# Performance work log

Measured on AMD Instinct MI355X. Metric: run time of the kernel, lower is better.

Reference implementation:

```python
import jax, jax.numpy as jnp
import numpy as np

COMMITMENT_COST = 0.25
NUM_EMBEDDINGS = 512
EMBEDDING_DIM = 64


def setup_inputs() -> dict:
    key = jax.random.key(0)
    k1, k2 = jax.random.split(key)
    inputs = jax.random.normal(k1, (64, EMBEDDING_DIM, 32, 32), dtype=jnp.float32)
    # nn.Embedding init: uniform(-1/K, 1/K)
    emb_w = jax.random.uniform(
        k2, (NUM_EMBEDDINGS, EMBEDDING_DIM), dtype=jnp.float32,
        minval=-1.0 / NUM_EMBEDDINGS, maxval=1.0 / NUM_EMBEDDINGS)
    return {"inputs": inputs, "emb_w": emb_w}


def reference(inputs, emb_w):
    sg = jax.lax.stop_gradient
    # NCHW -> NHWC
    x = jnp.transpose(inputs, (0, 2, 3, 1))          # [B, H, W, D]
    B, H, W, D = x.shape
    flat = x.reshape(-1, D)                          # [N, D]
    dist = (jnp.sum(flat * flat, axis=1, keepdims=True)
            + jnp.sum(emb_w * emb_w, axis=1)
            - 2.0 * jnp.dot(flat, emb_w.T))          # [N, K]
    idx = jnp.argmin(dist, axis=1)                   # [N]
    # one-hot @ emb_w is just a gather
    quantized = emb_w[idx].reshape(B, H, W, D)       # [B, H, W, D]
    e_latent_loss = jnp.mean((sg(quantized) - x) ** 2)
    q_latent_loss = jnp.mean((quantized - sg(x)) ** 2)
    loss = q_latent_loss + COMMITMENT_COST * e_latent_loss
    # straight-through estimator
    quantized_st = x + sg(quantized - x)
    out = jnp.transpose(quantized_st, (0, 3, 1, 2))  # back to NCHW
    return loss, out, idx[:, None]
```

## Files before the change

kernel.cpp:

```cpp
#include <hip/hip_runtime.h>


#define D_    64
#define HW_   1024
#define N_    65536
#define K_    512
#define M_    128
#define CH_   128
#define NCH_  4
#define NDTOT (N_ * K_ / 8)
#define SVST  132

__global__ __launch_bounds__(256, 2) void vq_main_kernel(const float* __restrict__ inp,
                                                         const float* __restrict__ emb,
                                                         float* __restrict__ out) {
    __shared__ float lds[17156];
    float* ldsx = lds;
    float* ldse = lds + 8192;
    float* nrm  = lds + 16384;
    float* sxs  = lds + 16896;
    int*   fi   = (int*)(lds + 17024);
    float* partial = lds + 17152;

    const int tid  = threadIdx.x;
    const int lane = tid & 63;
    const int wv   = tid >> 6;
    const int pg = (lane & 7) | ((wv & 1) << 3);
    const int kg = ((lane >> 3) & 7) | ((wv >> 1) << 3);

    const int n0  = blockIdx.x * M_;
    const int b   = n0 >> 10;
    const int hw0 = n0 & 1023;
    const float* xbase = inp + b * (D_ * HW_) + hw0;

#pragma unroll
    for (int i = 0; i < 8; ++i) {
        int q  = i * 256 + tid;
        int d  = q >> 5;
        int pq = q & 31;
        float4 v = *(const float4*)(xbase + d * HW_ + pq * 4);
        *(float4*)(ldsx + d * M_ + pq * 4) = v;
    }

#pragma unroll
    for (int h = 0; h < 2; ++h) {
        int k = h * 256 + tid;
        const float* e = emb + k * D_;
        float r[8];
#pragma unroll
        for (int j = 0; j < 8; ++j) r[j] = __fmul_rn(e[j], e[j]);
#pragma unroll
        for (int i = 1; i < 8; ++i)
#pragma unroll
            for (int j = 0; j < 8; ++j)
                r[j] = __fadd_rn(r[j], __fmul_rn(e[i * 8 + j], e[i * 8 + j]));
        nrm[k] = __fadd_rn(__fadd_rn(__fadd_rn(r[0], r[1]), __fadd_rn(r[2], r[3])),
                           __fadd_rn(__fadd_rn(r[4], r[5]), __fadd_rn(r[6], r[7])));
    }
    __syncthreads();

    if (tid < M_) {
        float r[8];
#pragma unroll
        for (int j = 0; j < 8; ++j) {
            float v = ldsx[j * M_ + tid];
            r[j] = __fmul_rn(v, v);
        }
#pragma unroll
        for (int i = 1; i < 8; ++i)
#pragma unroll
            for (int j = 0; j < 8; ++j) {
                float v = ldsx[(i * 8 + j) * M_ + tid];
                r[j] = __fadd_rn(r[j], __fmul_rn(v, v));
            }
        sxs[tid] = __fadd_rn(__fadd_rn(__fadd_rn(r[0], r[1]), __fadd_rn(r[2], r[3])),
                             __fadd_rn(__fadd_rn(r[4], r[5]), __fadd_rn(r[6], r[7])));
    }
    __syncthreads();

    float sxp[8];
#pragma unroll
    for (int pp = 0; pp < 8; ++pp) sxp[pp] = sxs[pg * 8 + pp];

    float runv[8];
    int   runi[8];
#pragma unroll
    for (int pp = 0; pp < 8; ++pp) { runv[pp] = 3.4e38f; runi[pp] = 0; }

    for (int c = 0; c < NCH_; ++c) {
        __syncthreads();
#pragma unroll
        for (int i = 0; i < 8; ++i) {
            int q  = i * 256 + tid;
            int kl = q & 127;
            int dq = q >> 7;
            float4 v = *(const float4*)(emb + (c * CH_ + kl) * D_ + dq * 4);
            ldse[(dq * 4 + 0) * CH_ + kl] = v.x;
            ldse[(dq * 4 + 1) * CH_ + kl] = v.y;
            ldse[(dq * 4 + 2) * CH_ + kl] = v.z;
            ldse[(dq * 4 + 3) * CH_ + kl] = v.w;
        }
        __syncthreads();

        float acc[8][8];
#pragma unroll
        for (int pp = 0; pp < 8; ++pp)
#pragma unroll
            for (int kk = 0; kk < 8; ++kk) acc[pp][kk] = 0.f;

#pragma unroll 2
        for (int d = 0; d < D_; ++d) {
            float4 xa = *(const float4*)(ldsx + d * M_ + pg * 8);
            float4 xb = *(const float4*)(ldsx + d * M_ + pg * 8 + 4);
            float4 ea = *(const float4*)(ldse + d * CH_ + kg * 8);
            float4 eb = *(const float4*)(ldse + d * CH_ + kg * 8 + 4);
            float xr[8] = {xa.x, xa.y, xa.z, xa.w, xb.x, xb.y, xb.z, xb.w};
            float er[8] = {ea.x, ea.y, ea.z, ea.w, eb.x, eb.y, eb.z, eb.w};
#pragma unroll
            for (int pp = 0; pp < 8; ++pp)
#pragma unroll
                for (int kk = 0; kk < 8; ++kk)
                    acc[pp][kk] = fmaf(xr[pp], er[kk], acc[pp][kk]);
        }

#pragma unroll
        for (int pp = 0; pp < 8; ++pp) {
            float sx = sxp[pp];
#pragma unroll
            for (int kk = 0; kk < 8; ++kk) {
                float nk = nrm[c * CH_ + kg * 8 + kk];
                float t1 = __fadd_rn(sx, nk);
                float v  = __fadd_rn(t1, -2.0f * acc[pp][kk]);
                if (v < runv[pp]) { runv[pp] = v; runi[pp] = c * CH_ + kg * 8 + kk; }
            }
        }
    }

    __syncthreads();
    float* sv = ldse;
    int*   si = (int*)(ldse + 16 * SVST);
#pragma unroll
    for (int pp = 0; pp < 8; ++pp) {
        sv[kg * SVST + pg * 8 + pp] = runv[pp];
        si[kg * SVST + pg * 8 + pp] = runi[pp];
    }
    __syncthreads();
    if (tid < M_) {
        float bv = 3.4e38f; int bi = 0x7fffffff;
#pragma unroll
        for (int g = 0; g < 16; ++g) {
            float v  = sv[g * SVST + tid];
            int   ii = si[g * SVST + tid];
            if (v < bv || (v == bv && ii < bi)) { bv = v; bi = ii; }
        }
        fi[tid] = bi;
        out[1 + NDTOT + n0 + tid] = (float)bi;
    }
    __syncthreads();

    const int h = tid >> 7;
    const int p = tid & 127;
    const int idx = fi[p];
    const float4* erow = (const float4*)(emb + idx * D_) + h * 8;
    float* obase = out + 1 + b * (D_ * HW_) + hw0 + p;
    float local = 0.f;
#pragma unroll
    for (int j = 0; j < 8; ++j) {
        float4 e4 = erow[j];
        int d0 = h * 32 + j * 4;
        float ev[4] = {e4.x, e4.y, e4.z, e4.w};
#pragma unroll
        for (int cc = 0; cc < 4; ++cc) {
            float xv = ldsx[(d0 + cc) * M_ + p];
            float df = ev[cc] - xv;
            local = fmaf(df, df, local);
            obase[(d0 + cc) * HW_] = ev[cc];
        }
    }
#pragma unroll
    for (int off = 32; off > 0; off >>= 1)
        local += __shfl_down(local, off, 64);
    if ((tid & 63) == 0) partial[tid >> 6] = local;
    __syncthreads();
    if (tid == 0) {
        float t = partial[0] + partial[1] + partial[2] + partial[3];
        atomicAdd(out, t * (1.25f / (float)NDTOT));
    }
}

extern "C" void kernel_launch(void* const* d_in, const int* in_sizes, int n_in,
                              void* d_out, int out_size, void* d_ws, size_t ws_size,
                              hipStream_t stream) {
    const float* inp = (const float*)d_in[0];
    const float* emb = (const float*)d_in[1];
    float* out = (float*)d_out;

    hipMemsetAsync(d_out, 0, sizeof(float), stream);
    vq_main_kernel<<<512, 256, 0, stream>>>(inp, emb, out);
}
```

Baseline: 138.5 us.

## Compute VQ distances with split-bf16 MFMA and refine near-ties exactly in fp32

Replaces the scalar fp32 FMA distance GEMM with bf16 MFMA 16x16x32 instructions. Inputs and codebook are split into hi/lo bf16 pairs (three products per tile) to approximate fp32 accuracy. A second MFMA pass finds candidate codes within a small margin of the approximate minimum and re-evaluates them with exact fp32 dot products, merged through 64-bit atomicCAS keys so the argmin matches the reference. Codebook fragments and norms are precomputed by two small prep kernels into device globals. This costs extra launches, a doubled MFMA pass, and a correctness dependence on the margin heuristic.

Result: faster. 133.6 us (-3.5%).

```diff
diff --git a/kernel.cpp b/kernel.cpp
--- a/kernel.cpp
+++ b/kernel.cpp
@@ -1,168 +1,281 @@
 #include <hip/hip_runtime.h>
 
 
-#define D_    64
-#define HW_   1024
-#define N_    65536
-#define K_    512
-#define M_    128
-#define CH_   128
-#define NCH_  4
-#define NDTOT (N_ * K_ / 8)
-#define SVST  132
+#define D_     64
+#define HW_    1024
+#define N_     65536
+#define K_     512
+#define NDTOT  4194304
+#define MARGIN 2e-4f
+
+typedef short v8s __attribute__((ext_vector_type(8)));
+typedef float v4f __attribute__((ext_vector_type(4)));
+
+__device__ float g_wsn[K_];
+__device__ short g_frag[K_ * D_ * 2];
+
+__device__ __forceinline__ unsigned short bf16rn(float f) {
+    unsigned int u = __float_as_uint(f);
+    u += 0x7fffu + ((u >> 16) & 1u);
+    return (unsigned short)(u >> 16);
+}
+__device__ __forceinline__ float bf16tof(unsigned short h) {
+    return __uint_as_float(((unsigned int)h) << 16);
+}
+
+__device__ __forceinline__ void exact_min(const float* xcolp, const float* __restrict__ emb,
+                                          int k, float sx, unsigned long long* keyp) {
+    const float* e = emb + k * D_;
+    float dot = 0.f;
+#pragma unroll 8
+    for (int d = 0; d < D_; ++d)
+        dot = fmaf(xcolp[d * HW_], e[d], dot);
+    float t1 = __fadd_rn(sx, g_wsn[k]);
+    float v  = fmaf(-2.0f, dot, t1);
+    unsigned long long nv =
+        (((unsigned long long)__float_as_uint(v)) << 32) | (unsigned int)k;
+    unsigned long long old = *keyp;
+    while (nv < old) {
+        unsigned long long assumed = old;
+        old = atomicCAS(keyp, assumed, nv);
+        if (old == assumed) break;
+    }
+}
+
+__global__ __launch_bounds__(256) void vq_prep_norm(const float* __restrict__ emb,
+                                                    float* __restrict__ out) {
+    int k = blockIdx.x * 256 + threadIdx.x;
+    if (k == 0) out[0] = 0.f;
+    if (k < K_) {
+        const float* e = emb + k * D_;
+        float r[8];
+#pragma unroll
+        for (int j = 0; j < 8; ++j) r[j] = __fmul_rn(e[j], e[j]);
+#pragma unroll
+        for (int i = 1; i < 8; ++i)
+#pragma unroll
+            for (int j = 0; j < 8; ++j)
+                r[j] = __fadd_rn(r[j], __fmul_rn(e[i * 8 + j], e[i * 8 + j]));
+        g_wsn[k] = __fadd_rn(__fadd_rn(__fadd_rn(r[0], r[1]), __fadd_rn(r[2], r[3])),
+                             __fadd_rn(__fadd_rn(r[4], r[5]), __fadd_rn(r[6], r[7])));
+    }
+}
+
+__global__ __launch_bounds__(256) void vq_prep_frag(const float* __restrict__ emb) {
+    const int t = blockIdx.x;
+    const int tid = threadIdx.x;
+    const int s = tid >> 7;
+    const int hl = (tid >> 6) & 1;
+    const int lane = tid & 63;
+    const int c = lane & 15, q = lane >> 4;
+    const float* e = emb + (t * 16 + c) * D_ + s * 32 + q * 8;
+    unsigned int u[4];
+#pragma unroll
+    for (int jp = 0; jp < 4; ++jp) {
+        float f0 = e[jp * 2], f1 = e[jp * 2 + 1];
+        unsigned short h0, h1;
+        if (hl == 0) { h0 = bf16rn(f0); h1 = bf16rn(f1); }
+        else {
+            h0 = bf16rn(f0 - bf16tof(bf16rn(f0)));
+            h1 = bf16rn(f1 - bf16tof(bf16rn(f1)));
+        }
+        u[jp] = (unsigned int)h0 | ((unsigned int)h1 << 16);
+    }
+    ((uint4*)g_frag)[(t * 4 + s * 2 + hl) * 64 + lane] =
+        make_uint4(u[0], u[1], u[2], u[3]);
+}
 
 __global__ __launch_bounds__(256, 2) void vq_main_kernel(const float* __restrict__ inp,
                                                          const float* __restrict__ emb,
                                                          float* __restrict__ out) {
-    __shared__ float lds[17156];
-    float* ldsx = lds;
-    float* ldse = lds + 8192;
-    float* nrm  = lds + 16384;
-    float* sxs  = lds + 16896;
-    int*   fi   = (int*)(lds + 17024);
-    float* partial = lds + 17152;
-
-    const int tid  = threadIdx.x;
+    __shared__ __align__(16) char smem[35344];
+    float* ldsx = (float*)smem;
+    v8s*   ldsB = (v8s*)smem;
+    float* sxs  = (float*)(smem + 32768);
+    float* m_   = (float*)(smem + 33280);
+    int*   ai_  = (int*)(smem + 33792);
+    unsigned long long* key_ = (unsigned long long*)(smem + 34304);
+    float* partial = (float*)(smem + 35328);
+
+    const int tid = threadIdx.x;
     const int lane = tid & 63;
-    const int wv   = tid >> 6;
-    const int pg = (lane & 7) | ((wv & 1) << 3);
-    const int kg = ((lane >> 3) & 7) | ((wv >> 1) << 3);
-
-    const int n0  = blockIdx.x * M_;
-    const int b   = n0 >> 10;
+    const int w = tid >> 6;
+    const int c = lane & 15, q = lane >> 4;
+
+    const int n0 = blockIdx.x * 128;
+    const int b = n0 >> 10;
     const int hw0 = n0 & 1023;
-    const float* xbase = inp + b * (D_ * HW_) + hw0;
+    const float* xg = inp + b * (D_ * HW_) + hw0;
 
 #pragma unroll
     for (int i = 0; i < 8; ++i) {
-        int q  = i * 256 + tid;
-        int d  = q >> 5;
-        int pq = q & 31;
-        float4 v = *(const float4*)(xbase + d * HW_ + pq * 4);
-        *(float4*)(ldsx + d * M_ + pq * 4) = v;
-    }
-
-#pragma unroll
-    for (int h = 0; h < 2; ++h) {
-        int k = h * 256 + tid;
-        const float* e = emb + k * D_;
+        int idx = i * 256 + tid;
+        int d = idx >> 5, pq = idx & 31;
+        *(float4*)(ldsx + d * 128 + pq * 4) = *(const float4*)(xg + d * HW_ + pq * 4);
+    }
+    __syncthreads();
+
+    if (tid < 128) {
         float r[8];
 #pragma unroll
-        for (int j = 0; j < 8; ++j) r[j] = __fmul_rn(e[j], e[j]);
+        for (int j = 0; j < 8; ++j) { float v = ldsx[j * 128 + tid]; r[j] = __fmul_rn(v, v); }
 #pragma unroll
         for (int i = 1; i < 8; ++i)
 #pragma unroll
-            for (int j = 0; j < 8; ++j)
-                r[j] = __fadd_rn(r[j], __fmul_rn(e[i * 8 + j], e[i * 8 + j]));
-        nrm[k] = __fadd_rn(__fadd_rn(__fadd_rn(r[0], r[1]), __fadd_rn(r[2], r[3])),
-                           __fadd_rn(__fadd_rn(r[4], r[5]), __fadd_rn(r[6], r[7])));
-    }
-    __syncthreads();
-
-    if (tid < M_) {
-        float r[8];
-#pragma unroll
-        for (int j = 0; j < 8; ++j) {
-            float v = ldsx[j * M_ + tid];
-            r[j] = __fmul_rn(v, v);
-        }
-#pragma unroll
-        for (int i = 1; i < 8; ++i)
-#pragma unroll
             for (int j = 0; j < 8; ++j) {
-                float v = ldsx[(i * 8 + j) * M_ + tid];
+                float v = ldsx[(i * 8 + j) * 128 + tid];
                 r[j] = __fadd_rn(r[j], __fmul_rn(v, v));
             }
         sxs[tid] = __fadd_rn(__fadd_rn(__fadd_rn(r[0], r[1]), __fadd_rn(r[2], r[3])),
                              __fadd_rn(__fadd_rn(r[4], r[5]), __fadd_rn(r[6], r[7])));
     }
-    __syncthreads();
-
-    float sxp[8];
-#pragma unroll
-    for (int pp = 0; pp < 8; ++pp) sxp[pp] = sxs[pg * 8 + pp];
-
-    float runv[8];
-    int   runi[8];
-#pragma unroll
-    for (int pp = 0; pp < 8; ++pp) { runv[pp] = 3.4e38f; runi[pp] = 0; }
-
-    for (int c = 0; c < NCH_; ++c) {
+
+    v8s ah[2][2], al[2][2];
+#pragma unroll
+    for (int T = 0; T < 2; ++T)
+#pragma unroll
+        for (int s = 0; s < 2; ++s) {
+            int pt = w * 32 + T * 16 + c;
+#pragma unroll
+            for (int j = 0; j < 8; ++j) {
+                float x = ldsx[(s * 32 + q * 8 + j) * 128 + pt];
+                float y = -2.0f * x;
+                unsigned short yh = bf16rn(y);
+                unsigned short yl = bf16rn(y - bf16tof(yh));
+                ah[T][s][j] = (short)yh;
+                al[T][s][j] = (short)yl;
+            }
+        }
+    __syncthreads();
+
+    float runv[2][4]; int runi[2][4];
+#pragma unroll
+    for (int T = 0; T < 2; ++T)
+#pragma unroll
+        for (int r = 0; r < 4; ++r) { runv[T][r] = 3.4e38f; runi[T][r] = 0; }
+
+    for (int ch = 0; ch < 4; ++ch) {
         __syncthreads();
-#pragma unroll
-        for (int i = 0; i < 8; ++i) {
-            int q  = i * 256 + tid;
-            int kl = q & 127;
-            int dq = q >> 7;
-            float4 v = *(const float4*)(emb + (c * CH_ + kl) * D_ + dq * 4);
-            ldse[(dq * 4 + 0) * CH_ + kl] = v.x;
-            ldse[(dq * 4 + 1) * CH_ + kl] = v.y;
-            ldse[(dq * 4 + 2) * CH_ + kl] = v.z;
-            ldse[(dq * 4 + 3) * CH_ + kl] = v.w;
+        {
+            const uint4* src = (const uint4*)(g_frag + ch * 16384);
+            uint4* dst = (uint4*)ldsB;
+#pragma unroll
+            for (int i = 0; i < 8; ++i) dst[i * 256 + tid] = src[i * 256 + tid];
         }
         __syncthreads();
-
-        float acc[8][8];
-#pragma unroll
-        for (int pp = 0; pp < 8; ++pp)
-#pragma unroll
-            for (int kk = 0; kk < 8; ++kk) acc[pp][kk] = 0.f;
-
-#pragma unroll 2
-        for (int d = 0; d < D_; ++d) {
-            float4 xa = *(const float4*)(ldsx + d * M_ + pg * 8);
-            float4 xb = *(const float4*)(ldsx + d * M_ + pg * 8 + 4);
-            float4 ea = *(const float4*)(ldse + d * CH_ + kg * 8);
-            float4 eb = *(const float4*)(ldse + d * CH_ + kg * 8 + 4);
-            float xr[8] = {xa.x, xa.y, xa.z, xa.w, xb.x, xb.y, xb.z, xb.w};
-            float er[8] = {ea.x, ea.y, ea.z, ea.w, eb.x, eb.y, eb.z, eb.w};
-#pragma unroll
-            for (int pp = 0; pp < 8; ++pp)
-#pragma unroll
-                for (int kk = 0; kk < 8; ++kk)
-                    acc[pp][kk] = fmaf(xr[pp], er[kk], acc[pp][kk]);
-        }
-
-#pragma unroll
-        for (int pp = 0; pp < 8; ++pp) {
-            float sx = sxp[pp];
-#pragma unroll
-            for (int kk = 0; kk < 8; ++kk) {
-                float nk = nrm[c * CH_ + kg * 8 + kk];
-                float t1 = __fadd_rn(sx, nk);
-                float v  = __fadd_rn(t1, -2.0f * acc[pp][kk]);
-                if (v < runv[pp]) { runv[pp] = v; runi[pp] = c * CH_ + kg * 8 + kk; }
-            }
-        }
-    }
-
-    __syncthreads();
-    float* sv = ldse;
-    int*   si = (int*)(ldse + 16 * SVST);
-#pragma unroll
-    for (int pp = 0; pp < 8; ++pp) {
-        sv[kg * SVST + pg * 8 + pp] = runv[pp];
-        si[kg * SVST + pg * 8 + pp] = runi[pp];
-    }
-    __syncthreads();
-    if (tid < M_) {
-        float bv = 3.4e38f; int bi = 0x7fffffff;
-#pragma unroll
-        for (int g = 0; g < 16; ++g) {
-            float v  = sv[g * SVST + tid];
-            int   ii = si[g * SVST + tid];
-            if (v < bv || (v == bv && ii < bi)) { bv = v; bi = ii; }
-        }
-        fi[tid] = bi;
-        out[1 + NDTOT + n0 + tid] = (float)bi;
-    }
-    __syncthreads();
-
-    const int h = tid >> 7;
-    const int p = tid & 127;
-    const int idx = fi[p];
+        float nk_arr[8];
+#pragma unroll
+        for (int ct = 0; ct < 8; ++ct) nk_arr[ct] = g_wsn[ch * 128 + ct * 16 + c];
+        for (int ct = 0; ct < 8; ++ct) {
+            const int kl = ch * 128 + ct * 16 + c;
+            const v8s* bp = ldsB + ct * 256 + lane;
+            v8s bh0 = bp[0], bl0 = bp[64], bh1 = bp[128], bl1 = bp[192];
+            float nk = nk_arr[ct];
+            v4f a0 = {nk, nk, nk, nk}, a1 = a0;
+            a0 = __builtin_amdgcn_mfma_f32_16x16x32_bf16(ah[0][0], bh0, a0, 0, 0, 0);
+            a0 = __builtin_amdgcn_mfma_f32_16x16x32_bf16(ah[0][0], bl0, a0, 0, 0, 0);
+            a0 = __builtin_amdgcn_mfma_f32_16x16x32_bf16(al[0][0], bh0, a0, 0, 0, 0);
+            a0 = __builtin_amdgcn_mfma_f32_16x16x32_bf16(ah[0][1], bh1, a0, 0, 0, 0);
+            a0 = __builtin_amdgcn_mfma_f32_16x16x32_bf16(ah[0][1], bl1, a0, 0, 0, 0);
+            a0 = __builtin_amdgcn_mfma_f32_16x16x32_bf16(al[0][1], bh1, a0, 0, 0, 0);
+            a1 = __builtin_amdgcn_mfma_f32_16x16x32_bf16(ah[1][0], bh0, a1, 0, 0, 0);
+            a1 = __builtin_amdgcn_mfma_f32_16x16x32_bf16(ah[1][0], bl0, a1, 0, 0, 0);
+            a1 = __builtin_amdgcn_mfma_f32_16x16x32_bf16(al[1][0], bh0, a1, 0, 0, 0);
+            a1 = __builtin_amdgcn_mfma_f32_16x16x32_bf16(ah[1][1], bh1, a1, 0, 0, 0);
+            a1 = __builtin_amdgcn_mfma_f32_16x16x32_bf16(ah[1][1], bl1, a1, 0, 0, 0);
+            a1 = __builtin_amdgcn_mfma_f32_16x16x32_bf16(al[1][1], bh1, a1, 0, 0, 0);
+#pragma unroll
+            for (int r = 0; r < 4; ++r) {
+                if (a0[r] < runv[0][r]) { runv[0][r] = a0[r]; runi[0][r] = kl; }
+                if (a1[r] < runv[1][r]) { runv[1][r] = a1[r]; runi[1][r] = kl; }
+            }
+        }
+    }
+
+#pragma unroll
+    for (int T = 0; T < 2; ++T)
+#pragma unroll
+        for (int r = 0; r < 4; ++r) {
+            float v = runv[T][r]; int i = runi[T][r];
+#pragma unroll
+            for (int off = 1; off < 16; off <<= 1) {
+                float ov = __shfl_xor(v, off, 64);
+                int   oi = __shfl_xor(i, off, 64);
+                if (ov < v || (ov == v && oi < i)) { v = ov; i = oi; }
+            }
+            if (c == 0) { int pt = w * 32 + T * 16 + q * 4 + r; m_[pt] = v; ai_[pt] = i; }
+        }
+    if (tid < 128) key_[tid] = 0xFFFFFFFFFFFFFFFFULL;
+    __syncthreads();
+
+    if (tid < 128) exact_min(xg + tid, emb, ai_[tid], sxs[tid], &key_[tid]);
+
+    float mm[2][4]; int aa[2][4];
+#pragma unroll
+    for (int T = 0; T < 2; ++T)
+#pragma unroll
+        for (int r = 0; r < 4; ++r) {
+            int pt = w * 32 + T * 16 + q * 4 + r;
+            mm[T][r] = m_[pt]; aa[T][r] = ai_[pt];
+        }
+
+    for (int ch = 0; ch < 4; ++ch) {
+        __syncthreads();
+        {
+            const uint4* src = (const uint4*)(g_frag + ch * 16384);
+            uint4* dst = (uint4*)ldsB;
+#pragma unroll
+            for (int i = 0; i < 8; ++i) dst[i * 256 + tid] = src[i * 256 + tid];
+        }
+        __syncthreads();
+        float nk_arr[8];
+#pragma unroll
+        for (int ct = 0; ct < 8; ++ct) nk_arr[ct] = g_wsn[ch * 128 + ct * 16 + c];
+        for (int ct = 0; ct < 8; ++ct) {
+            const int kl = ch * 128 + ct * 16 + c;
+            const v8s* bp = ldsB + ct * 256 + lane;
+            v8s bh0 = bp[0], bl0 = bp[64], bh1 = bp[128], bl1 = bp[192];
+            float nk = nk_arr[ct];
+            v4f a0 = {nk, nk, nk, nk}, a1 = a0;
+            a0 = __builtin_amdgcn_mfma_f32_16x16x32_bf16(ah[0][0], bh0, a0, 0, 0, 0);
+            a0 = __builtin_amdgcn_mfma_f32_16x16x32_bf16(ah[0][0], bl0, a0, 0, 0, 0);
+            a0 = __builtin_amdgcn_mfma_f32_16x16x32_bf16(al[0][0], bh0, a0, 0, 0, 0);
+            a0 = __builtin_amdgcn_mfma_f32_16x16x32_bf16(ah[0][1], bh1, a0, 0, 0, 0);
+            a0 = __builtin_amdgcn_mfma_f32_16x16x32_bf16(ah[0][1], bl1, a0, 0, 0, 0);
+            a0 = __builtin_amdgcn_mfma_f32_16x16x32_bf16(al[0][1], bh1, a0, 0, 0, 0);
+            a1 = __builtin_amdgcn_mfma_f32_16x16x32_bf16(ah[1][0], bh0, a1, 0, 0, 0);
+            a1 = __builtin_amdgcn_mfma_f32_16x16x32_bf16(ah[1][0], bl0, a1, 0, 0, 0);
+            a1 = __builtin_amdgcn_mfma_f32_16x16x32_bf16(al[1][0], bh0, a1, 0, 0, 0);
+            a1 = __builtin_amdgcn_mfma_f32_16x16x32_bf16(ah[1][1], bh1, a1, 0, 0, 0);
+            a1 = __builtin_amdgcn_mfma_f32_16x16x32_bf16(ah[1][1], bl1, a1, 0, 0, 0);
+            a1 = __builtin_amdgcn_mfma_f32_16x16x32_bf16(al[1][1], bh1, a1, 0, 0, 0);
+#pragma unroll
+            for (int r = 0; r < 4; ++r) {
+                if (a0[r] <= mm[0][r] + MARGIN && kl != aa[0][r]) {
+                    int pt = w * 32 + q * 4 + r;
+                    exact_min(xg + pt, emb, kl, sxs[pt], &key_[pt]);
+                }
+                if (a1[r] <= mm[1][r] + MARGIN && kl != aa[1][r]) {
+                    int pt = w * 32 + 16 + q * 4 + r;
+                    exact_min(xg + pt, emb, kl, sxs[pt], &key_[pt]);
+                }
+            }
+        }
+    }
+    __syncthreads();
+
+    if (tid < 128) {
+        unsigned int kf = (unsigned int)(key_[tid] & 0xffffffffULL);
+        ai_[tid] = (int)kf;
+        out[1 + NDTOT + n0 + tid] = (float)kf;
+    }
+    __syncthreads();
+
+    const int h = tid >> 7, p = tid & 127;
+    const int idx = ai_[p];
     const float4* erow = (const float4*)(emb + idx * D_) + h * 8;
-    float* obase = out + 1 + b * (D_ * HW_) + hw0 + p;
+    const float* xcol = xg + p;
+    float* ob = out + 1 + b * (D_ * HW_) + hw0 + p;
     float local = 0.f;
 #pragma unroll
     for (int j = 0; j < 8; ++j) {
@@ -171,10 +284,10 @@
         float ev[4] = {e4.x, e4.y, e4.z, e4.w};
 #pragma unroll
         for (int cc = 0; cc < 4; ++cc) {
-            float xv = ldsx[(d0 + cc) * M_ + p];
+            float xv = xcol[(d0 + cc) * HW_];
             float df = ev[cc] - xv;
             local = fmaf(df, df, local);
-            obase[(d0 + cc) * HW_] = ev[cc];
+            ob[(d0 + cc) * HW_] = ev[cc];
         }
     }
 #pragma unroll
@@ -195,6 +308,7 @@
     const float* emb = (const float*)d_in[1];
     float* out = (float*)d_out;
 
-    hipMemsetAsync(d_out, 0, sizeof(float), stream);
-    vq_main_kernel<<<512, 256, 0, stream>>>(inp, emb, out);
-}
+    vq_prep_norm<<<2, 256, 0, stream>>>(emb, out);
+    vq_prep_frag<<<32, 256, 0, stream>>>(emb);
+    vq_main_kernel<<<N_ / 128, 256, 0, stream>>>(inp, emb, out);
+}
```
